# Optimization experiments

Measured on AMD Instinct MI355X. Metric: run time of the kernel, lower is better.

The kernel has to match this reference:

```python
import jax, jax.numpy as jnp
import numpy as np

NH = 16   # num_heads
HD = 128  # head_dim
HS = 2048 # hidden_size
LI, LT = 2048, 512
MLP = 4 * HS


def _ln(x, s, b):
    m = jnp.mean(x, axis=-1, keepdims=True)
    v = jnp.var(x, axis=-1, keepdims=True)
    return (x - m) * jax.lax.rsqrt(v + 1e-6) * s + b


def _rms(x, s):
    return x * jax.lax.rsqrt(jnp.mean(x * x, axis=-1, keepdims=True) + 1e-6) * s


def _mod6(vec, w, b):
    a = (jax.nn.silu(vec) @ w + b)[:, None, :]
    return jnp.split(a, 6, axis=-1)  # shift1,scale1,gate1,shift2,scale2,gate2


def _rope(x, pe):
    B, H, L, D = x.shape
    xr = x.reshape(B, H, L, D // 2, 1, 2)
    return (pe[..., 0] * xr[..., 0] + pe[..., 1] * xr[..., 1]).reshape(B, H, L, D)


def _attention(q, k, v, pe):
    q = _rope(q, pe)
    k = _rope(k, pe)
    scores = jnp.einsum('bhqd,bhkd->bhqk', q, k) * (q.shape[-1] ** -0.5)
    p = jax.nn.softmax(scores, axis=-1)
    o = jnp.einsum('bhqk,bhkd->bhqd', p, v)
    B, H, L, D = o.shape
    return o.transpose(0, 2, 1, 3).reshape(B, L, H * D)


def _prenorm_qkv(x, shift, scale, ln_s, ln_b, qkv_w, qkv_b, qn, kn):
    xm = (1.0 + scale) * _ln(x, ln_s, ln_b) + shift
    y = xm @ qkv_w + qkv_b
    B, L, _ = y.shape
    y = y.reshape(B, L, 3, NH, HD).transpose(2, 0, 3, 1, 4)  # K B H L D
    q, k, v = y[0], y[1], y[2]
    return _rms(q, qn), _rms(k, kn), v


def _forward(img, txt, vec, pe,
             img_mod_w, img_mod_b, img_norm1_s, img_norm1_b, img_qkv_w, img_qkv_b,
             img_qn_s, img_kn_s, img_proj_w, img_proj_b, img_norm2_s, img_norm2_b,
             img_mlp_w1, img_mlp_b1, img_mlp_w2, img_mlp_b2,
             txt_mod_w, txt_mod_b, txt_norm1_s, txt_norm1_b, txt_qkv_w, txt_qkv_b,
             txt_qn_s, txt_kn_s, txt_proj_w, txt_proj_b, txt_norm2_s, txt_norm2_b,
             txt_mlp_w1, txt_mlp_b1, txt_mlp_w2, txt_mlp_b2):
    i_sh1, i_sc1, i_g1, i_sh2, i_sc2, i_g2 = _mod6(vec, img_mod_w, img_mod_b)
    t_sh1, t_sc1, t_g1, t_sh2, t_sc2, t_g2 = _mod6(vec, txt_mod_w, txt_mod_b)

    iq, ik, iv = _prenorm_qkv(img, i_sh1, i_sc1, img_norm1_s, img_norm1_b,
                              img_qkv_w, img_qkv_b, img_qn_s, img_kn_s)
    tq, tk, tv = _prenorm_qkv(txt, t_sh1, t_sc1, txt_norm1_s, txt_norm1_b,
                              txt_qkv_w, txt_qkv_b, txt_qn_s, txt_kn_s)

    q = jnp.concatenate((tq, iq), axis=2)
    k = jnp.concatenate((tk, ik), axis=2)
    v = jnp.concatenate((tv, iv), axis=2)
    attn = _attention(q, k, v, pe)  # [B, LT+LI, HS]
    Lt = txt.shape[1]
    txt_attn, img_attn = attn[:, :Lt], attn[:, Lt:]

    img = img + i_g1 * (img_attn @ img_proj_w + img_proj_b)
    img_h = (1.0 + i_sc2) * _ln(img, img_norm2_s, img_norm2_b) + i_sh2
    img = img + i_g2 * (jax.nn.gelu(img_h @ img_mlp_w1 + img_mlp_b1) @ img_mlp_w2 + img_mlp_b2)

    txt = txt + t_g1 * (txt_attn @ txt_proj_w + txt_proj_b)
    txt_h = (1.0 + t_sc2) * _ln(txt, txt_norm2_s, txt_norm2_b) + t_sh2
    txt = txt + t_g2 * (jax.nn.gelu(txt_h @ txt_mlp_w1 + txt_mlp_b1) @ txt_mlp_w2 + txt_mlp_b2)
    return img, txt


def setup_inputs() -> dict:
    key = jax.random.key(0)
    ki = iter(jax.random.split(key, 48))
    def n(shape, s=0.02):
        return jax.random.normal(next(ki), shape, jnp.float32) * s
    d = {
        'img': jax.random.normal(next(ki), (1, LI, HS), jnp.float32),
        'txt': jax.random.normal(next(ki), (1, LT, HS), jnp.float32),
        'vec': jax.random.normal(next(ki), (1, HS), jnp.float32),
        'pe': jax.random.normal(next(ki), (1, 1, LT + LI, HD // 2, 2, 2), jnp.float32),
    }
    for p in ('img', 'txt'):
        d[p + '_mod_w'] = n((HS, 6 * HS)); d[p + '_mod_b'] = jnp.zeros((6 * HS,), jnp.float32)
        d[p + '_norm1_s'] = jnp.ones((HS,), jnp.float32); d[p + '_norm1_b'] = jnp.zeros((HS,), jnp.float32)
        d[p + '_qkv_w'] = n((HS, 3 * HS)); d[p + '_qkv_b'] = jnp.zeros((3 * HS,), jnp.float32)
        d[p + '_qn_s'] = jnp.ones((HD,), jnp.float32); d[p + '_kn_s'] = jnp.ones((HD,), jnp.float32)
        d[p + '_proj_w'] = n((HS, HS)); d[p + '_proj_b'] = jnp.zeros((HS,), jnp.float32)
        d[p + '_norm2_s'] = jnp.ones((HS,), jnp.float32); d[p + '_norm2_b'] = jnp.zeros((HS,), jnp.float32)
        d[p + '_mlp_w1'] = n((HS, MLP)); d[p + '_mlp_b1'] = jnp.zeros((MLP,), jnp.float32)
        d[p + '_mlp_w2'] = n((MLP, HS)); d[p + '_mlp_b2'] = jnp.zeros((HS,), jnp.float32)
    return d


def reference(img, txt, vec, pe,
              img_mod_w, img_mod_b, img_norm1_s, img_norm1_b, img_qkv_w, img_qkv_b,
              img_qn_s, img_kn_s, img_proj_w, img_proj_b, img_norm2_s, img_norm2_b,
              img_mlp_w1, img_mlp_b1, img_mlp_w2, img_mlp_b2,
              txt_mod_w, txt_mod_b, txt_norm1_s, txt_norm1_b, txt_qkv_w, txt_qkv_b,
              txt_qn_s, txt_kn_s, txt_proj_w, txt_proj_b, txt_norm2_s, txt_norm2_b,
              txt_mlp_w1, txt_mlp_b1, txt_mlp_w2, txt_mlp_b2):
    return _forward(img, txt, vec, pe,
                    img_mod_w, img_mod_b, img_norm1_s, img_norm1_b, img_qkv_w, img_qkv_b,
                    img_qn_s, img_kn_s, img_proj_w, img_proj_b, img_norm2_s, img_norm2_b,
                    img_mlp_w1, img_mlp_b1, img_mlp_w2, img_mlp_b2,
                    txt_mod_w, txt_mod_b, txt_norm1_s, txt_norm1_b, txt_qkv_w, txt_qkv_b,
                    txt_qn_s, txt_kn_s, txt_proj_w, txt_proj_b, txt_norm2_s, txt_norm2_b,
                    txt_mlp_w1, txt_mlp_b1, txt_mlp_w2, txt_mlp_b2)
```

## Files before the change

kernel.cpp:

```cpp
#include <hip/hip_runtime.h>
#include <hip/hip_bf16.h>
#include <math.h>

typedef __bf16 bf16;
typedef __bf16 bf16x2 __attribute__((ext_vector_type(2)));
typedef __bf16 bf16x8 __attribute__((ext_vector_type(8)));
typedef float f32x4 __attribute__((ext_vector_type(4)));

#define HS 2048
#define NH 16
#define HD 128
#define LT 512
#define LI 2048
#define LQ 2560
#define MLP_D 8192
#define SPLIT 4
#define KVS (LQ / SPLIT)
#define KVBLK 32
#define NTILES (KVS / KVBLK)

__device__ __forceinline__ f32x4 mfma16(bf16x8 a, bf16x8 b, f32x4 c) {
  return __builtin_amdgcn_mfma_f32_16x16x32_bf16(a, b, c, 0, 0, 0);
}

__device__ __forceinline__ void gl_lds16(const bf16* g, bf16* l) {
  __builtin_amdgcn_global_load_lds((const __attribute__((address_space(1))) void*)g,
                                   (__attribute__((address_space(3))) void*)l, 16, 0, 0);
}

__global__ void k_silu(const float* __restrict__ v, float* __restrict__ s) {
  int i = blockIdx.x * 256 + threadIdx.x;
  float x = v[i];
  s[i] = x / (1.f + expf(-x));
}

__global__ __launch_bounds__(256) void k_mod_partial(
    const float* __restrict__ s, const float* __restrict__ w_txt,
    const float* __restrict__ w_img, float* __restrict__ part) {
  int strm = blockIdx.x / 48;
  int n = (blockIdx.x % 48) * 256 + threadIdx.x;
  const float* w = strm ? w_img : w_txt;
  int k0 = blockIdx.y * 256;
  __shared__ float sl[256];
  sl[threadIdx.x] = s[k0 + threadIdx.x];
  __syncthreads();
  float acc = 0.f;
  for (int k = 0; k < 256; k++)
    acc += sl[k] * w[(size_t)(k0 + k) * 12288 + n];
  part[((size_t)blockIdx.y * 2 + strm) * 12288 + n] = acc;
}

__global__ __launch_bounds__(256) void k_mod_reduce(
    const float* __restrict__ part, const float* __restrict__ b_txt,
    const float* __restrict__ b_img, float* __restrict__ mod) {
  int strm = blockIdx.x / 48;
  int n = (blockIdx.x % 48) * 256 + threadIdx.x;
  float acc = strm ? b_img[n] : b_txt[n];
  for (int kc = 0; kc < 8; kc++)
    acc += part[((size_t)kc * 2 + strm) * 12288 + n];
  mod[(size_t)strm * 12288 + n] = acc;
}

__global__ __launch_bounds__(256) void k_transpose_cvt(
    const float* __restrict__ src, bf16* __restrict__ dst, int R, int C) {
  __shared__ float t[64][65];
  int tx = threadIdx.x & 63, ty = threadIdx.x >> 6;
  int c0 = blockIdx.x * 64, r0 = blockIdx.y * 64;
  for (int i = 0; i < 64; i += 4)
    t[ty + i][tx] = src[(size_t)(r0 + ty + i) * C + c0 + tx];
  __syncthreads();
#pragma unroll
  for (int j = 0; j < 2; j++) {
    int c = (threadIdx.x >> 3) + j * 32;
    int gg = (threadIdx.x & 7) * 8;
    bf16x8 ov;
#pragma unroll
    for (int k = 0; k < 8; k++) ov[k] = (bf16)t[gg + k][c];
    *(bf16x8*)(dst + (size_t)(c0 + c) * R + r0 + gg) = ov;
  }
}

__global__ __launch_bounds__(256) void k_ln_mod(
    const float* __restrict__ x0, const float* __restrict__ x1,
    const float* __restrict__ ls0, const float* __restrict__ lb0,
    const float* __restrict__ ls1, const float* __restrict__ lb1,
    const float* __restrict__ mod0, const float* __restrict__ mod1,
    int shidx, int scidx, bf16* __restrict__ out) {
  int r = blockIdx.x;
  int strm = r >= LT;
  const float* x = strm ? (x1 + (size_t)(r - LT) * HS) : (x0 + (size_t)r * HS);
  const float* ls = strm ? ls1 : ls0;
  const float* lb = strm ? lb1 : lb0;
  const float* md = strm ? mod1 : mod0;
  const float* sh = md + (size_t)shidx * HS;
  const float* sc = md + (size_t)scidx * HS;
  int t = threadIdx.x;
  float4 a = ((const float4*)x)[t * 2];
  float4 b = ((const float4*)x)[t * 2 + 1];
  float xv[8] = {a.x, a.y, a.z, a.w, b.x, b.y, b.z, b.w};
  float sum = 0.f, sq = 0.f;
#pragma unroll
  for (int j = 0; j < 8; j++) { sum += xv[j]; sq += xv[j] * xv[j]; }
#pragma unroll
  for (int m = 32; m; m >>= 1) { sum += __shfl_xor(sum, m); sq += __shfl_xor(sq, m); }
  __shared__ float red[8];
  int lane = t & 63, wid = t >> 6;
  if (!lane) { red[wid] = sum; red[wid + 4] = sq; }
  __syncthreads();
  float ts = red[0] + red[1] + red[2] + red[3];
  float tq = red[4] + red[5] + red[6] + red[7];
  float mean = ts * (1.f / HS);
  float var = tq * (1.f / HS) - mean * mean;
  float inv = rsqrtf(var + 1e-6f);
  int c0 = t * 8;
  bf16x8 ov;
#pragma unroll
  for (int j = 0; j < 8; j++) {
    int c = c0 + j;
    float v = ((xv[j] - mean) * inv * ls[c] + lb[c]) * (1.f + sc[c]) + sh[c];
    ov[j] = (bf16)v;
  }
  *(bf16x8*)(out + (size_t)r * HS + c0) = ov;
}

template <int MODE>
__global__ __launch_bounds__(256) void k_gemm(
    const bf16* __restrict__ A, int K, int N, int Ksz,
    const bf16* __restrict__ BT0, const bf16* __restrict__ BT1,
    const float* __restrict__ bias0, const float* __restrict__ bias1,
    void* __restrict__ out0, void* __restrict__ out1) {
  __shared__ bf16 As[2][128 * 32];
  __shared__ bf16 Bs[2][128 * 32];
  int tid = threadIdx.x;
  int bn = blockIdx.x, bm = blockIdx.y;
  int strm = (bm * 128) >= LT;
  int lm = bm * 128 - strm * LT;
  const bf16* BT = strm ? BT1 : BT0;
  int lane = tid & 63, wid = tid >> 6;
  int wr = wid >> 1, wc = wid & 1;
  int sr = tid >> 2;
  int scol = ((tid & 3) ^ (sr & 3)) * 8;
  const bf16* Ag = A + (size_t)(bm * 128 + sr) * K + scol;
  const bf16* Bg = BT + (size_t)(bn * 128 + sr) * K + scol;
  int kbeg = MODE == 4 ? blockIdx.z * Ksz : 0;
  int nk = Ksz / 32;
  auto stage = [&](int buf, int ks) {
    int k0 = kbeg + ks * 32;
    gl_lds16(Ag + k0, &As[buf][wid * 512]);
    gl_lds16(Ag + (size_t)64 * K + k0, &As[buf][2048 + wid * 512]);
    gl_lds16(Bg + k0, &Bs[buf][wid * 512]);
    gl_lds16(Bg + (size_t)64 * K + k0, &Bs[buf][2048 + wid * 512]);
  };
  f32x4 acc[4][4] = {};
  int r16 = lane & 15, g = lane >> 4;
  int fslot = (g ^ (r16 & 3)) * 8;
  stage(0, 0);
  int cur = 0;
  for (int ks = 0; ks < nk; ks++) {
    __syncthreads();
    if (ks + 1 < nk) stage(cur ^ 1, ks + 1);
    bf16x8 af[4], bfr[4];
#pragma unroll
    for (int m = 0; m < 4; m++)
      af[m] = *(const bf16x8*)&As[cur][(wr * 64 + m * 16 + r16) * 32 + fslot];
#pragma unroll
    for (int n = 0; n < 4; n++)
      bfr[n] = *(const bf16x8*)&Bs[cur][(wc * 64 + n * 16 + r16) * 32 + fslot];
#pragma unroll
    for (int m = 0; m < 4; m++)
#pragma unroll
      for (int n = 0; n < 4; n++)
        acc[m][n] = mfma16(af[m], bfr[n], acc[m][n]);
    cur ^= 1;
  }
  int col = lane & 15, rb = (lane >> 4) * 4;
  const float* bias = strm ? bias1 : bias0;
  float* part = MODE == 4 ? (float*)out0 + (size_t)blockIdx.z * LQ * N : nullptr;
#pragma unroll
  for (int m = 0; m < 4; m++) {
#pragma unroll
    for (int n = 0; n < 4; n++) {
      int gn = bn * 128 + wc * 64 + n * 16 + col;
      float bv = MODE == 4 ? 0.f : bias[gn];
#pragma unroll
      for (int r = 0; r < 4; r++) {
        int lr = wr * 64 + m * 16 + rb + r;
        float v = acc[m][n][r] + bv;
        if (MODE == 0) {
          ((bf16*)(strm ? out1 : out0))[(size_t)(lm + lr) * N + gn] = (bf16)v;
        } else if (MODE == 2) {
          float u2 = 1.5957691216057308f * (v + 0.044715f * v * v * v);
          float ge = v / (1.f + __expf(-u2));
          ((bf16*)(strm ? out1 : out0))[(size_t)(lm + lr) * N + gn] = (bf16)ge;
        } else {
          part[(size_t)(bm * 128 + lr) * N + gn] = v;
        }
      }
    }
  }
}

template <int S>
__global__ __launch_bounds__(256) void k_skcomb(
    const float* __restrict__ part, int N,
    const float* __restrict__ bias0, const float* __restrict__ bias1,
    const float* __restrict__ gate0, const float* __restrict__ gate1,
    const float* __restrict__ res0, const float* __restrict__ res1,
    float* __restrict__ out0, float* __restrict__ out1) {
  int gid = blockIdx.x * 256 + threadIdx.x;
  int nv = N >> 2;
  int row = gid / nv, cv = gid - row * nv;
  int strm = row >= LT;
  int lrow = row - strm * LT;
  const float* bias = strm ? bias1 : bias0;
  const float* gate = strm ? gate1 : gate0;
  const float* res = strm ? res1 : res0;
  float* out = strm ? out1 : out0;
  int c = cv * 4;
  float4 acc = *(const float4*)(bias + c);
#pragma unroll
  for (int s = 0; s < S; s++) {
    float4 p = *(const float4*)(part + ((size_t)s * LQ + row) * N + c);
    acc.x += p.x; acc.y += p.y; acc.z += p.z; acc.w += p.w;
  }
  float4 g = *(const float4*)(gate + c);
  float4 r = *(const float4*)(res + (size_t)lrow * N + c);
  float4 o = {r.x + g.x * acc.x, r.y + g.y * acc.y, r.z + g.z * acc.z, r.w + g.w * acc.w};
  *(float4*)(out + (size_t)lrow * N + c) = o;
}

__global__ __launch_bounds__(256) void k_qkv_post(
    const bf16* __restrict__ y, const float* __restrict__ pe,
    const float* __restrict__ qn0, const float* __restrict__ kn0,
    const float* __restrict__ qn1, const float* __restrict__ kn1,
    bf16* __restrict__ qh, bf16* __restrict__ kh) {
  int wv = (int)((blockIdx.x * 256 + threadIdx.x) >> 6);
  int lane = threadIdx.x & 63;
  int head = wv / LQ, l = wv - head * LQ;
  const bf16* yr = y + (size_t)l * (3 * HS) + head * HD;
  float q0 = (float)yr[2 * lane], q1 = (float)yr[2 * lane + 1];
  float k0 = (float)yr[HS + 2 * lane], k1 = (float)yr[HS + 2 * lane + 1];
  float sqs = q0 * q0 + q1 * q1, sks = k0 * k0 + k1 * k1;
#pragma unroll
  for (int m = 1; m < 64; m <<= 1) { sqs += __shfl_xor(sqs, m); sks += __shfl_xor(sks, m); }
  float rq = rsqrtf(sqs * (1.f / HD) + 1e-6f);
  float rk = rsqrtf(sks * (1.f / HD) + 1e-6f);
  int strm = l >= LT;
  const float* qn = strm ? qn1 : qn0;
  const float* kn = strm ? kn1 : kn0;
  float e0 = q0 * rq * qn[2 * lane], e1 = q1 * rq * qn[2 * lane + 1];
  float f0 = k0 * rk * kn[2 * lane], f1 = k1 * rk * kn[2 * lane + 1];
  float4 p = *(const float4*)(pe + ((size_t)l * 64 + lane) * 4);
  const float scl = 0.08838834764831845f;
  size_t qi = ((size_t)head * LQ + l) * HD + 2 * lane;
  bf16x2 qv = {(bf16)((p.x * e0 + p.y * e1) * scl), (bf16)((p.z * e0 + p.w * e1) * scl)};
  bf16x2 kv = {(bf16)(p.x * f0 + p.y * f1), (bf16)(p.z * f0 + p.w * f1)};
  *(bf16x2*)(qh + qi) = qv;
  *(bf16x2*)(kh + qi) = kv;
}

__global__ __launch_bounds__(256) void k_vtrans(const bf16* __restrict__ y,
                                                bf16* __restrict__ vT) {
  __shared__ bf16 t[32][34];
  int head = blockIdx.y >> 2, dt = blockIdx.y & 3;
  int tx = threadIdx.x & 31, ty = threadIdx.x >> 5;
  int l0 = blockIdx.x * 32, d0 = dt * 32;
  for (int i = 0; i < 32; i += 8)
    t[ty + i][tx] = y[(size_t)(l0 + ty + i) * (3 * HS) + 2 * HS + head * HD + d0 + tx];
  __syncthreads();
  for (int i = 0; i < 32; i += 8)
    vT[(size_t)(head * HD + d0 + ty + i) * LQ + l0 + tx] = t[tx][ty + i];
}

__global__ __launch_bounds__(256, 4) void k_attn(
    const bf16* __restrict__ Q, const bf16* __restrict__ Kh,
    const bf16* __restrict__ VT, bf16* __restrict__ Op, float* __restrict__ ml) {
  __shared__ bf16 Ks[2][KVBLK * 128];
  __shared__ bf16 Vs[2][128 * KVBLK];
  __shared__ bf16 P[4][16 * 34];
  int tid = threadIdx.x, lane = tid & 63, w = tid >> 6;
  int b = blockIdx.x;
  int qb = b % 40;
  int split = (b / 40) % SPLIT;
  int head = b / (40 * SPLIT);
  int qr = qb * 64 + w * 16;
  int r16 = lane & 15, g = lane >> 4;
  const bf16* qp = Q + ((size_t)head * LQ + qr + r16) * HD + g * 8;
  bf16x8 qf[4];
#pragma unroll
  for (int c = 0; c < 4; c++) qf[c] = *(const bf16x8*)(qp + c * 32);
  f32x4 O[8] = {};
  float mr[4], lr[4];
#pragma unroll
  for (int i = 0; i < 4; i++) { mr[i] = -1e30f; lr[i] = 0.f; }
  bf16* pl = &P[w][0];
  const bf16* kbase = Kh + ((size_t)head * LQ + split * KVS) * HD;
  const bf16* vbase = VT + (size_t)head * HD * LQ + split * KVS;
  int krow0 = w * 8 + (lane >> 4);
  int kslot = lane & 15;
  int vrow0 = w * 32 + (lane >> 2);
  int vslot = lane & 3;
  auto stage = [&](int buf, int t) {
    int kv0 = t * KVBLK;
#pragma unroll
    for (int i = 0; i < 2; i++) {
      int krow = krow0 + i * 4;
      gl_lds16(kbase + (size_t)(kv0 + krow) * HD + ((kslot ^ (krow & 7)) << 3),
               &Ks[buf][(w * 8 + i * 4) * 128]);
      int vrow = vrow0 + i * 16;
      gl_lds16(vbase + (size_t)vrow * LQ + kv0 + ((vslot ^ (vrow & 3)) << 3),
               &Vs[buf][(w * 32 + i * 16) * KVBLK]);
    }
  };
  stage(0, 0);
  int cur = 0;
  for (int t = 0; t < NTILES; t++) {
    __syncthreads();
    if (t + 1 < NTILES) stage(cur ^ 1, t + 1);
    const bf16* ks = &Ks[cur][0];
    const bf16* vs = &Vs[cur][0];
    f32x4 S0 = {}, S1 = {};
    int sw = (r16 & 7);
#pragma unroll
    for (int c = 0; c < 4; c++) {
      int slot = ((4 * c + g) ^ sw) << 3;
      bf16x8 ka = *(const bf16x8*)&ks[r16 * 128 + slot];
      bf16x8 kb = *(const bf16x8*)&ks[(16 + r16) * 128 + slot];
      S0 = mfma16(qf[c], ka, S0);
      S1 = mfma16(qf[c], kb, S1);
    }
    float alpha[4];
#pragma unroll
    for (int i = 0; i < 4; i++) {
      float mx = fmaxf(S0[i], S1[i]);
#pragma unroll
      for (int m = 8; m; m >>= 1) mx = fmaxf(mx, __shfl_xor(mx, m));
      float mn = fmaxf(mr[i], mx);
      float p0 = __expf(S0[i] - mn), p1 = __expf(S1[i] - mn);
      float rs = p0 + p1;
#pragma unroll
      for (int m = 8; m; m >>= 1) rs += __shfl_xor(rs, m);
      alpha[i] = __expf(mr[i] - mn);
      lr[i] = lr[i] * alpha[i] + rs;
      mr[i] = mn;
      pl[(4 * g + i) * 34 + r16] = (bf16)p0;
      pl[(4 * g + i) * 34 + 16 + r16] = (bf16)p1;
    }
    bf16x8 pf = *(const bf16x8*)&pl[r16 * 34 + g * 8];
    int vsl = (g ^ (r16 & 3)) * 8;
#pragma unroll
    for (int n = 0; n < 8; n++) {
      f32x4 o = O[n];
#pragma unroll
      for (int i = 0; i < 4; i++) o[i] *= alpha[i];
      bf16x8 vf = *(const bf16x8*)&vs[(n * 16 + r16) * KVBLK + vsl];
      O[n] = mfma16(pf, vf, o);
    }
    cur ^= 1;
  }
  const int NL = NH * LQ;
  bf16* op = Op + (size_t)split * NL * HD;
#pragma unroll
  for (int n = 0; n < 8; n++)
#pragma unroll
    for (int i = 0; i < 4; i++)
      op[((size_t)head * LQ + qr + 4 * g + i) * HD + n * 16 + r16] = (bf16)O[n][i];
  if (r16 == 0) {
#pragma unroll
    for (int i = 0; i < 4; i++) {
      int idx = head * LQ + qr + 4 * g + i;
      ml[(size_t)(split * 2 + 0) * NL + idx] = mr[i];
      ml[(size_t)(split * 2 + 1) * NL + idx] = lr[i];
    }
  }
}

__global__ __launch_bounds__(256) void k_attn_combine(
    const bf16* __restrict__ Op, const float* __restrict__ ml, bf16* __restrict__ out) {
  int lane = threadIdx.x & 63, w = threadIdx.x >> 6;
  int row = blockIdx.x * 4 + w;
  int head = row / LQ, l = row - head * LQ;
  const int NL = NH * LQ;
  float ms[SPLIT], ls[SPLIT], m = -1e30f;
#pragma unroll
  for (int s = 0; s < SPLIT; s++) {
    ms[s] = ml[(size_t)(s * 2) * NL + row];
    ls[s] = ml[(size_t)(s * 2 + 1) * NL + row];
    m = fmaxf(m, ms[s]);
  }
  float wsum = 0.f, wgt[SPLIT];
#pragma unroll
  for (int s = 0; s < SPLIT; s++) { wgt[s] = __expf(ms[s] - m); wsum += wgt[s] * ls[s]; }
  float inv = 1.f / wsum;
  size_t oi = (size_t)row * HD + 2 * lane;
  float a0 = 0.f, a1 = 0.f;
#pragma unroll
  for (int s = 0; s < SPLIT; s++) {
    bf16x2 v = *(const bf16x2*)(Op + (size_t)s * NL * HD + oi);
    a0 += wgt[s] * (float)v[0];
    a1 += wgt[s] * (float)v[1];
  }
  bf16x2 ov = {(bf16)(a0 * inv), (bf16)(a1 * inv)};
  *(bf16x2*)(out + (size_t)l * HS + head * HD + 2 * lane) = ov;
}

extern "C" void kernel_launch(void* const* d_in, const int* in_sizes, int n_in,
                              void* d_out, int out_size, void* d_ws, size_t ws_size,
                              hipStream_t stream) {
  const float* img = (const float*)d_in[0];
  const float* txt = (const float*)d_in[1];
  const float* vec = (const float*)d_in[2];
  const float* pe = (const float*)d_in[3];
#define PARAM(i) ((const float*)d_in[i])

  char* ws = (char*)d_ws;
  size_t off = 0;
  auto alloc = [&](size_t b) { void* p = ws + off; off += (b + 255) & ~(size_t)255; return p; };
  float* silu_s = (float*)alloc((size_t)HS * 4);
  float* mpart = (float*)alloc((size_t)8 * 2 * 12288 * 4);
  float* mod = (float*)alloc((size_t)2 * 6 * HS * 4);
  bf16* qkvT0 = (bf16*)alloc((size_t)3 * HS * HS * 2);
  bf16* qkvT1 = (bf16*)alloc((size_t)3 * HS * HS * 2);
  bf16* projT0 = (bf16*)alloc((size_t)HS * HS * 2);
  bf16* projT1 = (bf16*)alloc((size_t)HS * HS * 2);
  bf16* mlp1T0 = (bf16*)alloc((size_t)MLP_D * HS * 2);
  bf16* mlp1T1 = (bf16*)alloc((size_t)MLP_D * HS * 2);
  bf16* mlp2T0 = (bf16*)alloc((size_t)HS * MLP_D * 2);
  bf16* mlp2T1 = (bf16*)alloc((size_t)HS * MLP_D * 2);
  bf16* xm = (bf16*)alloc((size_t)LQ * HS * 2);
  bf16* y = (bf16*)alloc((size_t)LQ * 3 * HS * 2);
  bf16* qh = (bf16*)alloc((size_t)NH * LQ * HD * 2);
  bf16* kh = (bf16*)alloc((size_t)NH * LQ * HD * 2);
  bf16* vT = (bf16*)alloc((size_t)NH * HD * LQ * 2);
  bf16* attnb = (bf16*)alloc((size_t)LQ * HS * 2);
  float* x2 = (float*)alloc((size_t)LQ * HS * 4);
  bf16* xm2 = (bf16*)alloc((size_t)LQ * HS * 2);
  bf16* h = (bf16*)alloc((size_t)LQ * MLP_D * 2);
  float* ml = (float*)alloc((size_t)2 * SPLIT * NH * LQ * 4);
  bf16* Op = h;
  float* skpart = (float*)xm;
  (void)ws_size; (void)in_sizes; (void)n_in; (void)out_size;

  const float* t_mod = mod;
  const float* i_mod = mod + 6 * HS;

  k_silu<<<HS / 256, 256, 0, stream>>>(vec, silu_s);
  k_mod_partial<<<dim3(96, 8), 256, 0, stream>>>(silu_s, PARAM(20), PARAM(4), mpart);
  k_mod_reduce<<<96, 256, 0, stream>>>(mpart, PARAM(21), PARAM(5), mod);

  k_transpose_cvt<<<dim3(3 * HS / 64, HS / 64), 256, 0, stream>>>(PARAM(24), qkvT0, HS, 3 * HS);
  k_transpose_cvt<<<dim3(3 * HS / 64, HS / 64), 256, 0, stream>>>(PARAM(8), qkvT1, HS, 3 * HS);
  k_transpose_cvt<<<dim3(HS / 64, HS / 64), 256, 0, stream>>>(PARAM(28), projT0, HS, HS);
  k_transpose_cvt<<<dim3(HS / 64, HS / 64), 256, 0, stream>>>(PARAM(12), projT1, HS, HS);
  k_transpose_cvt<<<dim3(MLP_D / 64, HS / 64), 256, 0, stream>>>(PARAM(32), mlp1T0, HS, MLP_D);
  k_transpose_cvt<<<dim3(MLP_D / 64, HS / 64), 256, 0, stream>>>(PARAM(16), mlp1T1, HS, MLP_D);
  k_transpose_cvt<<<dim3(HS / 64, MLP_D / 64), 256, 0, stream>>>(PARAM(34), mlp2T0, MLP_D, HS);
  k_transpose_cvt<<<dim3(HS / 64, MLP_D / 64), 256, 0, stream>>>(PARAM(18), mlp2T1, MLP_D, HS);

  k_ln_mod<<<LQ, 256, 0, stream>>>(txt, img, PARAM(22), PARAM(23), PARAM(6), PARAM(7),
                                   t_mod, i_mod, 0, 1, xm);

  k_gemm<0><<<dim3(3 * HS / 128, LQ / 128), 256, 0, stream>>>(
      xm, HS, 3 * HS, HS, qkvT0, qkvT1, PARAM(25), PARAM(9), y, y + (size_t)LT * 3 * HS);

  k_qkv_post<<<NH * LQ / 4, 256, 0, stream>>>(y, pe, PARAM(26), PARAM(27), PARAM(10), PARAM(11),
                                              qh, kh);
  k_vtrans<<<dim3(LQ / 32, NH * 4), 256, 0, stream>>>(y, vT);

  k_attn<<<NH * SPLIT * 40, 256, 0, stream>>>(qh, kh, vT, Op, ml);
  k_attn_combine<<<NH * LQ / 4, 256, 0, stream>>>(Op, ml, attnb);

  k_gemm<4><<<dim3(HS / 128, LQ / 128, 2), 256, 0, stream>>>(
      attnb, HS, HS, HS / 2, projT0, projT1, nullptr, nullptr, skpart, nullptr);
  k_skcomb<2><<<LQ * HS / 4 / 256, 256, 0, stream>>>(
      skpart, HS, PARAM(29), PARAM(13), t_mod + 2 * HS, i_mod + 2 * HS, txt, img,
      x2, x2 + (size_t)LT * HS);

  k_ln_mod<<<LQ, 256, 0, stream>>>(x2, x2 + (size_t)LT * HS, PARAM(30), PARAM(31), PARAM(14),
                                   PARAM(15), t_mod, i_mod, 3, 4, xm2);

  k_gemm<2><<<dim3(MLP_D / 128, LQ / 128), 256, 0, stream>>>(
      xm2, HS, MLP_D, HS, mlp1T0, mlp1T1, PARAM(33), PARAM(17), h, h + (size_t)LT * MLP_D);

  float* out_img = (float*)d_out;
  float* out_txt = (float*)d_out + (size_t)LI * HS;
  k_gemm<4><<<dim3(HS / 128, LQ / 128, 4), 256, 0, stream>>>(
      h, MLP_D, HS, MLP_D / 4, mlp2T0, mlp2T1, nullptr, nullptr, skpart, nullptr);
  k_skcomb<4><<<LQ * HS / 4 / 256, 256, 0, stream>>>(
      skpart, HS, PARAM(35), PARAM(19), t_mod + 5 * HS, i_mod + 5 * HS, x2,
      x2 + (size_t)LT * HS, out_txt, out_img);
}
```

Measured before the change: 822.8 us.

## Transpose attention MFMAs, use exp2 softmax with lazy rescale, drop LDS P staging

Swaps the MFMA operand order so each lane owns one query row. Row max and sum then need only two cross-lane shuffles, and P is moved into the PV operand layout with register shuffles instead of a round trip through shared memory. The log2(e) factor is folded into the Q scale so exp2f can be used, and O is rescaled only when the running max grows by more than 8 (FA4-style lazy rescaling). Occupancy is raised to 5 blocks and output stores are vectorised. The cost is extra shuffle traffic, and the lazy rescale lets exponents reach up to 2^8 before renormalisation, which bf16 P must tolerate.

Result: faster. 763.1 us (-7.3%).

```diff
diff --git a/kernel.cpp b/kernel.cpp
--- a/kernel.cpp
+++ b/kernel.cpp
@@ -4,6 +4,7 @@
 
 typedef __bf16 bf16;
 typedef __bf16 bf16x2 __attribute__((ext_vector_type(2)));
+typedef __bf16 bf16x4 __attribute__((ext_vector_type(4)));
 typedef __bf16 bf16x8 __attribute__((ext_vector_type(8)));
 typedef float f32x4 __attribute__((ext_vector_type(4)));
 
@@ -251,7 +252,7 @@
   float e0 = q0 * rq * qn[2 * lane], e1 = q1 * rq * qn[2 * lane + 1];
   float f0 = k0 * rk * kn[2 * lane], f1 = k1 * rk * kn[2 * lane + 1];
   float4 p = *(const float4*)(pe + ((size_t)l * 64 + lane) * 4);
-  const float scl = 0.08838834764831845f;
+  const float scl = 0.12751744f;
   size_t qi = ((size_t)head * LQ + l) * HD + 2 * lane;
   bf16x2 qv = {(bf16)((p.x * e0 + p.y * e1) * scl), (bf16)((p.z * e0 + p.w * e1) * scl)};
   bf16x2 kv = {(bf16)(p.x * f0 + p.y * f1), (bf16)(p.z * f0 + p.w * f1)};
@@ -272,12 +273,11 @@
     vT[(size_t)(head * HD + d0 + ty + i) * LQ + l0 + tx] = t[tx][ty + i];
 }
 
-__global__ __launch_bounds__(256, 4) void k_attn(
+__global__ __launch_bounds__(256, 5) void k_attn(
     const bf16* __restrict__ Q, const bf16* __restrict__ Kh,
     const bf16* __restrict__ VT, bf16* __restrict__ Op, float* __restrict__ ml) {
   __shared__ bf16 Ks[2][KVBLK * 128];
   __shared__ bf16 Vs[2][128 * KVBLK];
-  __shared__ bf16 P[4][16 * 34];
   int tid = threadIdx.x, lane = tid & 63, w = tid >> 6;
   int b = blockIdx.x;
   int qb = b % 40;
@@ -290,10 +290,7 @@
 #pragma unroll
   for (int c = 0; c < 4; c++) qf[c] = *(const bf16x8*)(qp + c * 32);
   f32x4 O[8] = {};
-  float mr[4], lr[4];
-#pragma unroll
-  for (int i = 0; i < 4; i++) { mr[i] = -1e30f; lr[i] = 0.f; }
-  bf16* pl = &P[w][0];
+  float mr = -1e30f, lr = 0.f;
   const bf16* kbase = Kh + ((size_t)head * LQ + split * KVS) * HD;
   const bf16* vbase = VT + (size_t)head * HD * LQ + split * KVS;
   int krow0 = w * 8 + (lane >> 4);
@@ -314,6 +311,8 @@
   };
   stage(0, 0);
   int cur = 0;
+  int src0 = r16 + ((g & 1) << 5);
+  bool hiS = g >= 2;
   for (int t = 0; t < NTILES; t++) {
     __syncthreads();
     if (t + 1 < NTILES) stage(cur ^ 1, t + 1);
@@ -326,52 +325,65 @@
       int slot = ((4 * c + g) ^ sw) << 3;
       bf16x8 ka = *(const bf16x8*)&ks[r16 * 128 + slot];
       bf16x8 kb = *(const bf16x8*)&ks[(16 + r16) * 128 + slot];
-      S0 = mfma16(qf[c], ka, S0);
-      S1 = mfma16(qf[c], kb, S1);
+      S0 = mfma16(ka, qf[c], S0);
+      S1 = mfma16(kb, qf[c], S1);
     }
-    float alpha[4];
-#pragma unroll
-    for (int i = 0; i < 4; i++) {
-      float mx = fmaxf(S0[i], S1[i]);
-#pragma unroll
-      for (int m = 8; m; m >>= 1) mx = fmaxf(mx, __shfl_xor(mx, m));
-      float mn = fmaxf(mr[i], mx);
-      float p0 = __expf(S0[i] - mn), p1 = __expf(S1[i] - mn);
-      float rs = p0 + p1;
-#pragma unroll
-      for (int m = 8; m; m >>= 1) rs += __shfl_xor(rs, m);
-      alpha[i] = __expf(mr[i] - mn);
-      lr[i] = lr[i] * alpha[i] + rs;
-      mr[i] = mn;
-      pl[(4 * g + i) * 34 + r16] = (bf16)p0;
-      pl[(4 * g + i) * 34 + 16 + r16] = (bf16)p1;
+    float mx = fmaxf(fmaxf(fmaxf(S0[0], S0[1]), fmaxf(S0[2], S0[3])),
+                     fmaxf(fmaxf(S1[0], S1[1]), fmaxf(S1[2], S1[3])));
+    mx = fmaxf(mx, __shfl_xor(mx, 16));
+    mx = fmaxf(mx, __shfl_xor(mx, 32));
+    bool keep = __all(mx <= mr + 8.f);
+    float alpha = 1.f;
+    if (!keep) {
+      float mn = fmaxf(mr, mx);
+      alpha = exp2f(mr - mn);
+      mr = mn;
     }
-    bf16x8 pf = *(const bf16x8*)&pl[r16 * 34 + g * 8];
+    float p0 = exp2f(S0[0] - mr), p1 = exp2f(S0[1] - mr);
+    float p2 = exp2f(S0[2] - mr), p3 = exp2f(S0[3] - mr);
+    float p4 = exp2f(S1[0] - mr), p5 = exp2f(S1[1] - mr);
+    float p6 = exp2f(S1[2] - mr), p7 = exp2f(S1[3] - mr);
+    float rs = ((p0 + p1) + (p2 + p3)) + ((p4 + p5) + (p6 + p7));
+    rs += __shfl_xor(rs, 16);
+    rs += __shfl_xor(rs, 32);
+    lr = fmaf(lr, alpha, rs);
+    bf16x2 a0 = {(bf16)p0, (bf16)p1}, a1 = {(bf16)p2, (bf16)p3};
+    bf16x2 b0 = {(bf16)p4, (bf16)p5}, b1 = {(bf16)p6, (bf16)p7};
+    int A0 = *(int*)&a0, A1 = *(int*)&a1, B0 = *(int*)&b0, B1 = *(int*)&b1;
+    int x0a = __shfl(A0, src0), x0b = __shfl(B0, src0);
+    int x1a = __shfl(A1, src0), x1b = __shfl(B1, src0);
+    int x2a = __shfl(A0, src0 + 16), x2b = __shfl(B0, src0 + 16);
+    int x3a = __shfl(A1, src0 + 16), x3b = __shfl(B1, src0 + 16);
+    union { int u[4]; bf16x8 v; } pu;
+    pu.u[0] = hiS ? x0b : x0a;
+    pu.u[1] = hiS ? x1b : x1a;
+    pu.u[2] = hiS ? x2b : x2a;
+    pu.u[3] = hiS ? x3b : x3a;
+    bf16x8 pf = pu.v;
+    if (!keep) {
+#pragma unroll
+      for (int n = 0; n < 8; n++) O[n] *= alpha;
+    }
     int vsl = (g ^ (r16 & 3)) * 8;
 #pragma unroll
     for (int n = 0; n < 8; n++) {
-      f32x4 o = O[n];
-#pragma unroll
-      for (int i = 0; i < 4; i++) o[i] *= alpha[i];
       bf16x8 vf = *(const bf16x8*)&vs[(n * 16 + r16) * KVBLK + vsl];
-      O[n] = mfma16(pf, vf, o);
+      O[n] = mfma16(vf, pf, O[n]);
     }
     cur ^= 1;
   }
   const int NL = NH * LQ;
   bf16* op = Op + (size_t)split * NL * HD;
-#pragma unroll
-  for (int n = 0; n < 8; n++)
-#pragma unroll
-    for (int i = 0; i < 4; i++)
-      op[((size_t)head * LQ + qr + 4 * g + i) * HD + n * 16 + r16] = (bf16)O[n][i];
-  if (r16 == 0) {
-#pragma unroll
-    for (int i = 0; i < 4; i++) {
-      int idx = head * LQ + qr + 4 * g + i;
-      ml[(size_t)(split * 2 + 0) * NL + idx] = mr[i];
-      ml[(size_t)(split * 2 + 1) * NL + idx] = lr[i];
-    }
+  size_t rowbase = ((size_t)head * LQ + qr + r16) * HD + 4 * g;
+#pragma unroll
+  for (int n = 0; n < 8; n++) {
+    bf16x4 ov = {(bf16)O[n][0], (bf16)O[n][1], (bf16)O[n][2], (bf16)O[n][3]};
+    *(bf16x4*)(op + rowbase + n * 16) = ov;
+  }
+  if (g == 0) {
+    int idx = head * LQ + qr + r16;
+    ml[(size_t)(split * 2 + 0) * NL + idx] = mr;
+    ml[(size_t)(split * 2 + 1) * NL + idx] = lr;
   }
 }
 
@@ -390,7 +402,7 @@
   }
   float wsum = 0.f, wgt[SPLIT];
 #pragma unroll
-  for (int s = 0; s < SPLIT; s++) { wgt[s] = __expf(ms[s] - m); wsum += wgt[s] * ls[s]; }
+  for (int s = 0; s < SPLIT; s++) { wgt[s] = exp2f(ms[s] - m); wsum += wgt[s] * ls[s]; }
   float inv = 1.f / wsum;
   size_t oi = (size_t)row * HD + 2 * lane;
   float a0 = 0.f, a1 = 0.f;
```
